# Kernel optimization log

Measured on AMD Instinct MI355X. Metric: run time of the kernel, lower is better.

Reference implementation:

```python
import jax, jax.numpy as jnp
import numpy as np

EPS = 1e-6
HQ, HKV, HD = 16, 4, 64   # num_q_heads, num_kv_heads, head_dim
TOPK = 2                  # num_exp_tokens
B, S, H, E, I = 2, 1024, 1024, 8, 2048


def _rms(x, w):
    return x * jax.lax.rsqrt(jnp.mean(x * x, -1, keepdims=True) + EPS) * w


def _rope(x, cos, sin):
    # x: [B,S,h,D]; cos/sin: [S,D/2]
    x1, x2 = jnp.split(x, 2, axis=-1)
    c = cos[None, :, None, :]
    s = sin[None, :, None, :]
    return jnp.concatenate([x1 * c - x2 * s, x1 * s + x2 * c], axis=-1)


def setup_inputs() -> dict:
    key = jax.random.key(0)
    ks = jax.random.split(key, 12)
    w = lambda k, sh: jax.random.normal(k, sh, jnp.float32) * 0.02
    return {
        "x": jax.random.normal(ks[0], (B, S, H), jnp.float32),
        "freq": jax.random.uniform(ks[1], (S, HD // 2), jnp.float32) * 6.28,
        "norm1_w": jnp.ones((H,), jnp.float32),
        "norm2_w": jnp.ones((H,), jnp.float32),
        "wq": w(ks[2], (H, HQ * HD)),
        "wk": w(ks[3], (H, HKV * HD)),
        "wv": w(ks[4], (H, HKV * HD)),
        "wo": w(ks[5], (HQ * HD, H)),
        "qn_w": jnp.ones((HD,), jnp.float32),
        "kn_w": jnp.ones((HD,), jnp.float32),
        "gate_w": w(ks[6], (H, E)),
        "w1": w(ks[7], (E, H, I)),
        "w2": w(ks[8], (E, I, H)),
        "w3": w(ks[9], (E, H, I)),
    }


def reference(x, freq, norm1_w, norm2_w, wq, wk, wv, wo, qn_w, kn_w,
              gate_w, w1, w2, w3):
    b, s, h = x.shape
    # ---- GQA attention with qk_norm + RoPE ----
    hn = _rms(x, norm1_w)
    q = (hn @ wq).reshape(b, s, HQ, HD)
    k = (hn @ wk).reshape(b, s, HKV, HD)
    v = (hn @ wv).reshape(b, s, HKV, HD)
    q = _rms(q, qn_w)
    k = _rms(k, kn_w)
    cos, sin = jnp.cos(freq), jnp.sin(freq)
    q = _rope(q, cos, sin)
    k = _rope(k, cos, sin)
    rep = HQ // HKV
    kr = jnp.repeat(k, rep, axis=2)  # [b,s,HQ,HD]
    vr = jnp.repeat(v, rep, axis=2)
    scores = jnp.einsum('bqhd,bkhd->bhqk', q, kr) * (HD ** -0.5)
    mask = jnp.tril(jnp.ones((s, s), bool))
    scores = jnp.where(mask, scores, jnp.finfo(scores.dtype).min)
    att = jax.nn.softmax(scores, axis=-1)
    y = jnp.einsum('bhqk,bkhd->bqhd', att, vr).reshape(b, s, HQ * HD) @ wo
    x = x + y

    # ---- Sparse MoE FFN (top-k softmax gate, SwiGLU experts) ----
    t = _rms(x, norm2_w).reshape(b * s, h)
    probs = jax.nn.softmax(t @ gate_w, axis=-1)          # [T,E]
    vals, idx = jax.lax.top_k(probs, TOPK)               # [T,k]
    vals = vals / jnp.sum(vals, -1, keepdims=True)       # renormalize top-k
    T = b * s
    combine = jnp.zeros((T, E), t.dtype).at[
        jnp.arange(T)[:, None], idx].add(vals)           # [T,E]
    u = jnp.einsum('th,ehi->eti', t, w1)
    g = jax.nn.silu(u) * jnp.einsum('th,ehi->eti', t, w3)
    ye = jnp.einsum('eti,eih->eth', g, w2)               # [E,T,H]
    moe = jnp.einsum('eth,te->th', ye, combine).reshape(b, s, h)
    return (x + moe, k, v)
```

## Files before the change

kernel.cpp:

```cpp
#include <hip/hip_runtime.h>
#include <hip/hip_bf16.h>

#define HQn 16
#define HKVn 4
#define HDn 64
#define Bn 2
#define Sn 1024
#define Hn 1024
#define En 8
#define In 2048
#define Tn 2048
#define EPSf 1e-6f

typedef __attribute__((ext_vector_type(8))) short bf16x8;
typedef __attribute__((ext_vector_type(4))) float f32x4;

__device__ __forceinline__ unsigned short f2bf(float f) {
  unsigned u = __float_as_uint(f);
  u += 0x7fffu + ((u >> 16) & 1u);
  return (unsigned short)(u >> 16);
}
__device__ __forceinline__ float bf2f(unsigned short u) {
  return __uint_as_float(((unsigned)u) << 16);
}
// ... 72 lines not shown
    unsigned short* __restrict__ outh, unsigned short* __restrict__ outl) {
  int row = blockIdx.x, tid = threadIdx.x;
  size_t off = (size_t)row * Hn + tid * 4;
  float4 v = *(const float4*)(x + off);
  float ss = v.x * v.x + v.y * v.y + v.z * v.z + v.w * v.w;
#pragma unroll
  for (int o = 32; o > 0; o >>= 1) ss += __shfl_xor(ss, o);
  __shared__ float ls[4];
  if ((tid & 63) == 0) ls[tid >> 6] = ss;
  __syncthreads();
  float tot = ls[0] + ls[1] + ls[2] + ls[3];
  float sc = rsqrtf(tot * (1.0f / Hn) + EPSf);
  float4 wv = *(const float4*)(w + tid * 4);
  float o0 = v.x * sc * wv.x, o1 = v.y * sc * wv.y;
  float o2 = v.z * sc * wv.z, o3 = v.w * sc * wv.w;
  ushort4 h4, l4;
  h4.x = f2bf(o0); l4.x = f2bf(o0 - bf2f(h4.x));
  h4.y = f2bf(o1); l4.y = f2bf(o1 - bf2f(h4.y));
  h4.z = f2bf(o2); l4.z = f2bf(o2 - bf2f(h4.z));
  h4.w = f2bf(o3); l4.w = f2bf(o3 - bf2f(h4.w));
  *(ushort4*)(outh + off) = h4;
  *(ushort4*)(outl + off) = l4;
}

__global__ __launch_bounds__(256) void k_resid_norm(
    const float* __restrict__ x, const float* __restrict__ y,
    const float* __restrict__ w, float* __restrict__ x2out,
    float* __restrict__ tout, unsigned short* __restrict__ tbf) {
  int row = blockIdx.x, tid = threadIdx.x;
  size_t off = (size_t)row * Hn + tid * 4;
  float4 xv = *(const float4*)(x + off);
  float4 yv = *(const float4*)(y + off);
  float4 s;
  s.x = xv.x + yv.x; s.y = xv.y + yv.y; s.z = xv.z + yv.z; s.w = xv.w + yv.w;
  *(float4*)(x2out + off) = s;
  float ss = s.x * s.x + s.y * s.y + s.z * s.z + s.w * s.w;
#pragma unroll
  for (int o = 32; o > 0; o >>= 1) ss += __shfl_xor(ss, o);
  __shared__ float ls[4];
  if ((tid & 63) == 0) ls[tid >> 6] = ss;
  __syncthreads();
  float tot = ls[0] + ls[1] + ls[2] + ls[3];
  float sc = rsqrtf(tot * (1.0f / Hn) + EPSf);
  float4 wv4 = *(const float4*)(w + tid * 4);
  float4 t4;
  t4.x = s.x * sc * wv4.x; t4.y = s.y * sc * wv4.y;
  t4.z = s.z * sc * wv4.z; t4.w = s.w * sc * wv4.w;
  *(float4*)(tout + off) = t4;
  ushort4 b4;
  b4.x = f2bf(t4.x); b4.y = f2bf(t4.y); b4.z = f2bf(t4.z); b4.w = f2bf(t4.w);
  *(ushort4*)(tbf + off) = b4;
}

template<int MT>
__global__ __launch_bounds__(256) void k_pgemm(
    const unsigned short* __restrict__ Ah, const unsigned short* __restrict__ Al,
    const unsigned short* __restrict__ Bth, const unsigned short* __restrict__ Btl,
    float* __restrict__ C, int N, int K) {
  constexpr int BM = MT * 32;
  __shared__ __align__(16) short smAh[BM * 32], smAl[BM * 32];
  __shared__ __align__(16) short smBh[4096], smBl[4096];
  int tid = threadIdx.x, wave = tid >> 6, lane = tid & 63;
  int n0 = blockIdx.x * 128, m0 = blockIdx.y * BM;
  int wm = wave >> 1, wn = wave & 1;
  int r0 = ((tid >> 6) << 4) | (tid & 15);
  int k0 = ((tid >> 4) & 3) * 8;
  int r1 = r0 + 64;
  const unsigned short* Ah0 = Ah + (size_t)(m0 + r0) * K + k0;
  const unsigned short* Al0 = Al + (size_t)(m0 + r0) * K + k0;
  const unsigned short* Bh0 = Bth + (size_t)(n0 + r0) * K + k0;
  const unsigned short* Bl0 = Btl + (size_t)(n0 + r0) * K + k0;
  const unsigned short* Bh1 = Bth + (size_t)(n0 + r1) * K + k0;
  const unsigned short* Bl1 = Btl + (size_t)(n0 + r1) * K + k0;
  short* dA0h = smAh + (size_t)(wave * 64) * 8;
  short* dA0l = smAl + (size_t)(wave * 64) * 8;
  short* dB0h = smBh + (size_t)(wave * 64) * 8;
  short* dB0l = smBl + (size_t)(wave * 64) * 8;
  short* dB1h = smBh + (size_t)(256 + wave * 64) * 8;
  short* dB1l = smBl + (size_t)(256 + wave * 64) * 8;
  const unsigned short* Ah1 = Ah0;
  const unsigned short* Al1 = Al0;
  short* dA1h = smAh;
  short* dA1l = smAl;
  if constexpr (MT == 4) {
    Ah1 = Ah + (size_t)(m0 + r1) * K + k0;
    Al1 = Al + (size_t)(m0 + r1) * K + k0;
    dA1h = smAh + (size_t)(256 + wave * 64) * 8;
    dA1l = smAl + (size_t)(256 + wave * 64) * 8;
  }
  f32x4 zf = {0.f, 0.f, 0.f, 0.f};
  f32x4 acc[MT][4];
#pragma unroll
  for (int i = 0; i < MT; i++)
#pragma unroll
    for (int j = 0; j < 4; j++) acc[i][j] = zf;
  for (int kb = 0; kb < K; kb += 32) {
    __syncthreads();
    gll16(Ah0 + kb, dA0h);
    gll16(Al0 + kb, dA0l);
    if constexpr (MT == 4) {
      gll16(Ah1 + kb, dA1h);
      gll16(Al1 + kb, dA1l);
    }
    gll16(Bh0 + kb, dB0h);
    gll16(Bl0 + kb, dB0l);
    gll16(Bh1 + kb, dB1h);
    gll16(Bl1 + kb, dB1l);
    __syncthreads();
    bf16x8 ah[MT], al[MT], bh[4], bl[4];
#pragma unroll
    for (int i = 0; i < MT; i++) {
      ah[i] = *(const bf16x8*)(smAh + ((wm * MT + i) * 64 + lane) * 8);
      al[i] = *(const bf16x8*)(smAl + ((wm * MT + i) * 64 + lane) * 8);
    }
#pragma unroll
    for (int j = 0; j < 4; j++) {
      bh[j] = *(const bf16x8*)(smBh + ((wn * 4 + j) * 64 + lane) * 8);
      bl[j] = *(const bf16x8*)(smBl + ((wn * 4 + j) * 64 + lane) * 8);
    }
#pragma unroll
    for (int i = 0; i < MT; i++)
#pragma unroll
      for (int j = 0; j < 4; j++) {
        acc[i][j] = __builtin_amdgcn_mfma_f32_16x16x32_bf16(ah[i], bh[j], acc[i][j], 0, 0, 0);
        acc[i][j] = __builtin_amdgcn_mfma_f32_16x16x32_bf16(ah[i], bl[j], acc[i][j], 0, 0, 0);
        acc[i][j] = __builtin_amdgcn_mfma_f32_16x16x32_bf16(al[i], bh[j], acc[i][j], 0, 0, 0);
      }
  }
  int cr = (lane >> 4) * 4, cc = lane & 15;
#pragma unroll
  for (int i = 0; i < MT; i++) {
    int row0 = m0 + (wm * MT + i) * 16 + cr;
#pragma unroll
    for (int j = 0; j < 4; j++) {
      int col = n0 + (wn * 4 + j) * 16 + cc;
#pragma unroll
      for (int r = 0; r < 4; r++)
        C[(size_t)(row0 + r) * N + col] = acc[i][j][r];
    }
  }
}

__global__ __launch_bounds__(256) void k_qkv_post(
    const float* __restrict__ qkv, const float* __restrict__ qn_w,
    const float* __restrict__ kn_w, const float* __restrict__ freq,
    float* __restrict__ q_t,
    unsigned short* __restrict__ kT8h, unsigned short* __restrict__ kT8l,
    unsigned short* __restrict__ vT8h, unsigned short* __restrict__ vT8l,
    float* __restrict__ k_out, float* __restrict__ v_out) {
  int gw = blockIdx.x * 4 + (threadIdx.x >> 6);
  int lane = threadIdx.x & 63;
  int token = gw / 24;
  int hh = gw % 24;
  int b = token / Sn, s = token % Sn;
  if (hh >= 20) {
    int h = hh - 20;
    float v = qkv[(size_t)token * 1536 + 1280 + h * HDn + lane];
    unsigned short hi = f2bf(v);
    unsigned short lo = f2bf(v - bf2f(hi));
    size_t vb = (((size_t)(b * HKVn + h) * 128 + (s >> 3)) * 64 + lane) * 8 + (s & 7);
    vT8h[vb] = hi; vT8l[vb] = lo;
    v_out[(size_t)token * (HKVn * HDn) + h * HDn + lane] = v;
    return;
  }
  bool isq = hh < 16;
  int h = isq ? hh : hh - 16;
  float val = isq ? qkv[(size_t)token * 1536 + h * HDn + lane]
                  : qkv[(size_t)token * 1536 + 1024 + h * HDn + lane];
  float ss = val * val;
#pragma unroll
  for (int o = 32; o > 0; o >>= 1) ss += __shfl_xor(ss, o);
  float scn = rsqrtf(ss * (1.0f / HDn) + EPSf);
  float w = isq ? qn_w[lane] : kn_w[lane];
  float xn = val * scn * w;
  float f = freq[(size_t)s * (HDn / 2) + (lane & 31)];
  float c = cosf(f), sn = sinf(f);
  float partner = __shfl_xor(xn, 32);
  float out = (lane < 32) ? (xn * c - partner * sn) : (partner * sn + xn * c);
  if (isq) {
    q_t[(((size_t)(b * HQn + h)) * Sn + s) * HDn + lane] = out;
  } else {
    unsigned short hi = f2bf(out);
    unsigned short lo = f2bf(out - bf2f(hi));
    size_t kb = (((size_t)(b * HKVn + h) * 8 + (lane >> 3)) * Sn + s) * 8 + (lane & 7);
    kT8h[kb] = hi; kT8l[kb] = lo;
// ... 154 lines not shown
    s[6] = fmaf(tv, g1.z, s[6]); s[7] = fmaf(tv, g1.w, s[7]);
  }
#pragma unroll
  for (int e = 0; e < 8; e++)
#pragma unroll
    for (int off = 32; off > 0; off >>= 1) s[e] += __shfl_xor(s[e], off);
  if (lane == 0) {
    float mx = s[0];
    for (int e = 1; e < 8; e++) mx = fmaxf(mx, s[e]);
    float p[8];
    for (int e = 0; e < 8; e++) p[e] = __expf(s[e] - mx);
    int e0 = 0;
    for (int e = 1; e < 8; e++) if (p[e] > p[e0]) e0 = e;
    int e1 = (e0 == 0) ? 1 : 0;
    for (int e = 0; e < 8; e++) if (e != e0 && p[e] > p[e1]) e1 = e;
    float v0 = p[e0], v1 = p[e1], inv = 1.f / (v0 + v1);
    idx[tok * 2] = e0; idx[tok * 2 + 1] = e1;
    val[tok * 2] = v0 * inv; val[tok * 2 + 1] = v1 * inv;
    atomicAdd(&cnt[e0], 1); atomicAdd(&cnt[e1], 1);
  }
}

__global__ void k_scan(const int* __restrict__ cnt, int* __restrict__ offs,
                       int* __restrict__ cursor) {
  if (threadIdx.x == 0) {
    int run = 0;
    for (int e = 0; e < En; e++) { offs[e] = run; cursor[e] = run; run += cnt[e]; }
  }
}

__global__ __launch_bounds__(256) void k_scatter(
    const int* __restrict__ idx, const float* __restrict__ val,
    int* __restrict__ cursor, int* __restrict__ tokl, float* __restrict__ wvl) {
  int t = blockIdx.x * 256 + threadIdx.x;
#pragma unroll
  for (int slot = 0; slot < 2; slot++) {
    int e = idx[t * 2 + slot];
    int pos = atomicAdd(&cursor[e], 1);
    tokl[pos] = t;
    wvl[pos] = val[t * 2 + slot];
  }
}

__global__ __launch_bounds__(256) void k_gather(
    const unsigned short* __restrict__ tb, const int* __restrict__ tokl,
    unsigned short* __restrict__ tg) {
  int r = blockIdx.x;
  int tk = tokl[r];
  const ushort4* s = (const ushort4*)(tb + (size_t)tk * Hn);
  ushort4* d = (ushort4*)(tg + (size_t)r * Hn);
  d[threadIdx.x] = s[threadIdx.x];
}

__global__ __launch_bounds__(256) void k_moe13(
    const unsigned short* __restrict__ tg, const unsigned short* __restrict__ w13t,
    unsigned short* __restrict__ ug, const int* __restrict__ cnt,
    const int* __restrict__ offs) {
  int e = blockIdx.z;
  int n_e = cnt[e];
  int mt = blockIdx.y;
  if (mt * 128 >= n_e) return;
  int base = offs[e];
  const unsigned short* A = tg + (size_t)(base + mt * 128) * Hn;
  const unsigned short* Bt = w13t + (size_t)e * (2 * In) * Hn;
  __shared__ __align__(16) short smA[4096];
  __shared__ __align__(16) short smB[4096];
  int tid = threadIdx.x;
  int wave = tid >> 6, lane = tid & 63;
  int n0 = blockIdx.x * 128;
  int wm = wave >> 1, wn = wave & 1;
  int s0 = tid, s1 = 256 + tid;
  int r0s = ((s0 >> 6) << 4) | (s0 & 15), k0s = ((s0 >> 4) & 3) * 8;
  int r1s = ((s1 >> 6) << 4) | (s1 & 15), k1s = ((s1 >> 4) & 3) * 8;
  const unsigned short* Ap0 = A + (size_t)r0s * Hn + k0s;
  const unsigned short* Ap1 = A + (size_t)r1s * Hn + k1s;
  const unsigned short* Bp0 = Bt + (size_t)(n0 + r0s) * Hn + k0s;
  const unsigned short* Bp1 = Bt + (size_t)(n0 + r1s) * Hn + k1s;
  short* lA0 = smA + (size_t)(wave * 64) * 8;
  short* lA1 = smA + (size_t)(256 + wave * 64) * 8;
  short* lB0 = smB + (size_t)(wave * 64) * 8;
  short* lB1 = smB + (size_t)(256 + wave * 64) * 8;
  f32x4 zf = {0.f, 0.f, 0.f, 0.f};
  f32x4 acc[4][4];
#pragma unroll
  for (int i = 0; i < 4; i++)
#pragma unroll
    for (int j = 0; j < 4; j++) acc[i][j] = zf;
  for (int kb = 0; kb < Hn; kb += 32) {
    __syncthreads();
    gll16(Ap0 + kb, lA0);
    gll16(Ap1 + kb, lA1);
    gll16(Bp0 + kb, lB0);
    gll16(Bp1 + kb, lB1);
    __syncthreads();
    bf16x8 af[4], bfr[4];
#pragma unroll
    for (int i = 0; i < 4; i++)
      af[i] = *(const bf16x8*)(smA + ((wm * 4 + i) * 64 + lane) * 8);
#pragma unroll
    for (int j = 0; j < 4; j++)
      bfr[j] = *(const bf16x8*)(smB + ((wn * 4 + j) * 64 + lane) * 8);
#pragma unroll
    for (int i = 0; i < 4; i++)
#pragma unroll
      for (int j = 0; j < 4; j++)
        acc[i][j] = __builtin_amdgcn_mfma_f32_16x16x32_bf16(af[i], bfr[j], acc[i][j], 0, 0, 0);
  }
  int cr = (lane >> 4) * 4, cc = lane & 15;
#pragma unroll
  for (int i = 0; i < 4; i++) {
    int lrow0 = (wm * 4 + i) * 16 + cr;
#pragma unroll
    for (int j = 0; j < 4; j++) {
      int ncol = n0 + (wn * 4 + j) * 16 + cc;
#pragma unroll
      for (int r = 0; r < 4; r++) {
        int rr = mt * 128 + lrow0 + r;
        if (rr < n_e)
          ug[(size_t)(base + rr) * (2 * In) + ncol] = f2bf(acc[i][j][r]);
      }
    }
  }
}

__global__ __launch_bounds__(256) void k_act(
    const unsigned short* __restrict__ ug, unsigned short* __restrict__ act) {
  size_t p = ((size_t)blockIdx.x * 256 + threadIdx.x) * 8;
  size_t r = p >> 11;
  int c = (int)(p & 2047);
  const ushort4* up = (const ushort4*)(ug + r * 4096 + c);
  const ushort4* gp = (const ushort4*)(ug + r * 4096 + 2048 + c);
  ushort4* ap = (ushort4*)(act + r * 2048 + c);
#pragma unroll
  for (int h = 0; h < 2; h++) {
    ushort4 uu = up[h], gg = gp[h];
    ushort4 oo;
    float u0 = bf2f(uu.x), u1 = bf2f(uu.y), u2 = bf2f(uu.z), u3 = bf2f(uu.w);
    oo.x = f2bf(u0 / (1.f + __expf(-u0)) * bf2f(gg.x));
    oo.y = f2bf(u1 / (1.f + __expf(-u1)) * bf2f(gg.y));
    oo.z = f2bf(u2 / (1.f + __expf(-u2)) * bf2f(gg.z));
    oo.w = f2bf(u3 / (1.f + __expf(-u3)) * bf2f(gg.w));
    ap[h] = oo;
  }
}

__global__ __launch_bounds__(256) void k_moe2(
    const unsigned short* __restrict__ act, const unsigned short* __restrict__ w2t,
    const int* __restrict__ cnt, const int* __restrict__ offs,
    const int* __restrict__ tokl, const float* __restrict__ wvl,
    float* __restrict__ out0) {
  int e = blockIdx.z;
  int n_e = cnt[e];
  int mt = blockIdx.y;
  if (mt * 128 >= n_e) return;
  int base = offs[e];
  __shared__ int ltok[128];
  __shared__ float lwv[128];
  int tid = threadIdx.x;
  if (tid < 128) {
    int rr = mt * 128 + tid;
    bool v = rr < n_e;
    ltok[tid] = v ? tokl[base + rr] : -1;
    lwv[tid] = v ? wvl[base + rr] : 0.f;
  }
  const unsigned short* A = act + (size_t)(base + mt * 128) * In;
  const unsigned short* Bt = w2t + (size_t)e * Hn * In;
  __shared__ __align__(16) short smA[4096];
  __shared__ __align__(16) short smB[4096];
  int wave = tid >> 6, lane = tid & 63;
  int n0 = blockIdx.x * 128;
  int wm = wave >> 1, wn = wave & 1;
  int s0 = tid, s1 = 256 + tid;
  int r0s = ((s0 >> 6) << 4) | (s0 & 15), k0s = ((s0 >> 4) & 3) * 8;
  int r1s = ((s1 >> 6) << 4) | (s1 & 15), k1s = ((s1 >> 4) & 3) * 8;
  const unsigned short* Ap0 = A + (size_t)r0s * In + k0s;
  const unsigned short* Ap1 = A + (size_t)r1s * In + k1s;
  const unsigned short* Bp0 = Bt + (size_t)(n0 + r0s) * In + k0s;
  const unsigned short* Bp1 = Bt + (size_t)(n0 + r1s) * In + k1s;
  short* lA0 = smA + (size_t)(wave * 64) * 8;
  short* lA1 = smA + (size_t)(256 + wave * 64) * 8;
  short* lB0 = smB + (size_t)(wave * 64) * 8;
  short* lB1 = smB + (size_t)(256 + wave * 64) * 8;
  f32x4 zf = {0.f, 0.f, 0.f, 0.f};
  f32x4 acc[4][4];
#pragma unroll
  for (int i = 0; i < 4; i++)
#pragma unroll
    for (int j = 0; j < 4; j++) acc[i][j] = zf;
  for (int kb = 0; kb < In; kb += 32) {
    __syncthreads();
    gll16(Ap0 + kb, lA0);
    gll16(Ap1 + kb, lA1);
    gll16(Bp0 + kb, lB0);
    gll16(Bp1 + kb, lB1);
    __syncthreads();
    bf16x8 af[4], bfr[4];
#pragma unroll
    for (int i = 0; i < 4; i++)
      af[i] = *(const bf16x8*)(smA + ((wm * 4 + i) * 64 + lane) * 8);
#pragma unroll
    for (int j = 0; j < 4; j++)
      bfr[j] = *(const bf16x8*)(smB + ((wn * 4 + j) * 64 + lane) * 8);
#pragma unroll
    for (int i = 0; i < 4; i++)
#pragma unroll
      for (int j = 0; j < 4; j++)
        acc[i][j] = __builtin_amdgcn_mfma_f32_16x16x32_bf16(af[i], bfr[j], acc[i][j], 0, 0, 0);
  }
  int cr = (lane >> 4) * 4, cc = lane & 15;
#pragma unroll
  for (int i = 0; i < 4; i++) {
    int lrow0 = (wm * 4 + i) * 16 + cr;
#pragma unroll
    for (int j = 0; j < 4; j++) {
      int ncol = n0 + (wn * 4 + j) * 16 + cc;
#pragma unroll
      for (int r = 0; r < 4; r++) {
        int lrow = lrow0 + r;
        int tk = ltok[lrow];
        if (tk >= 0)
          atomicAdd(out0 + (size_t)tk * Hn + ncol, lwv[lrow] * acc[i][j][r]);
      }
    }
  }
}

extern "C" void kernel_launch(void* const* d_in, const int* in_sizes, int n_in,
                              void* d_out, int out_size, void* d_ws, size_t ws_size,
                              hipStream_t stream) {
  (void)in_sizes; (void)n_in; (void)out_size; (void)ws_size;
  const float* x      = (const float*)d_in[0];
  const float* freq   = (const float*)d_in[1];
  const float* n1w    = (const float*)d_in[2];
  const float* n2w    = (const float*)d_in[3];
  const float* wq     = (const float*)d_in[4];
  const float* wk     = (const float*)d_in[5];
  const float* wvp    = (const float*)d_in[6];
  const float* wo     = (const float*)d_in[7];
  const float* qn_w   = (const float*)d_in[8];
  const float* kn_w   = (const float*)d_in[9];
  const float* gate_w = (const float*)d_in[10];
  const float* w1     = (const float*)d_in[11];
  const float* w2     = (const float*)d_in[12];
  const float* w3     = (const float*)d_in[13];

  float* out0  = (float*)d_out;
  float* k_out = out0 + (size_t)Tn * Hn;
  float* v_out = k_out + (size_t)Tn * HKVn * HDn;

  char* wsb = (char*)d_ws;
  unsigned short* w13t = (unsigned short*)(wsb + 0);
  unsigned short* w2t  = (unsigned short*)(wsb + 67108864);
  unsigned short* tbf  = (unsigned short*)(wsb + 100663296);
  unsigned short* tg   = (unsigned short*)(wsb + 104857600);
  unsigned short* wqkvt_h = (unsigned short*)(wsb + 113246208);
  unsigned short* wqkvt_l = (unsigned short*)(wsb + 116391936);
  unsigned short* wot_h   = (unsigned short*)(wsb + 119537664);
  unsigned short* wot_l   = (unsigned short*)(wsb + 121634816);
  unsigned short* act  = (unsigned short*)(wsb + 113246208);
  unsigned short* hnh  = (unsigned short*)(wsb + 130023424);
  unsigned short* hnl  = (unsigned short*)(wsb + 134217728);
  float* qkv_raw = (float*)(wsb + 138412032);
  float* q_t   = (float*)(wsb + 150994944);
  unsigned short* kT8h = (unsigned short*)(wsb + 159383552);
  unsigned short* kT8l = (unsigned short*)(wsb + 160432128);
  unsigned short* vT8h = (unsigned short*)(wsb + 161480704);
  unsigned short* vT8l = (unsigned short*)(wsb + 162529280);
  unsigned short* ug = (unsigned short*)(wsb + 130023424);
  unsigned short* yh = (unsigned short*)(wsb + 163577856);
  unsigned short* yl = (unsigned short*)(wsb + 167772160);
  float* y2    = (float*)(wsb + 171966464);
  float* t_norm = (float*)(wsb + 150994944);
  char*  rtr   = wsb + 180355072;
  int*   idxb   = (int*)(rtr);
  float* valb   = (float*)(rtr + 16384);
  int*   cnt    = (int*)(rtr + 32768);
  int*   offs   = (int*)(rtr + 32768 + 128);
  int*   cursor = (int*)(rtr + 32768 + 256);
  int*   tokl   = (int*)(rtr + 32768 + 384);
  float* wvl    = (float*)(rtr + 32768 + 384 + 16384);

  k_tcvt<<<dim3(32, 16, 8), 256, 0, stream>>>(w1, w13t, 1024, 2048,
                                              (size_t)1024 * 2048, (size_t)4096 * 1024);
  k_tcvt<<<dim3(32, 16, 8), 256, 0, stream>>>(w3, w13t + (size_t)2048 * 1024, 1024, 2048,
                                              (size_t)1024 * 2048, (size_t)4096 * 1024);
  k_tcvt<<<dim3(16, 32, 8), 256, 0, stream>>>(w2, w2t, 2048, 1024,
                                              (size_t)2048 * 1024, (size_t)1024 * 2048);
  k_tcvt2<<<dim3(16, 16), 256, 0, stream>>>(wq, wqkvt_h, wqkvt_l, 1024, 1024);
  k_tcvt2<<<dim3(4, 16), 256, 0, stream>>>(wk, wqkvt_h + (size_t)1024 * 1024,
                                           wqkvt_l + (size_t)1024 * 1024, 1024, 256);
  k_tcvt2<<<dim3(4, 16), 256, 0, stream>>>(wvp, wqkvt_h + (size_t)1280 * 1024,
                                           wqkvt_l + (size_t)1280 * 1024, 1024, 256);
  k_tcvt2<<<dim3(16, 16), 256, 0, stream>>>(wo, wot_h, wot_l, 1024, 1024);

  hipMemsetAsync(cnt, 0, 8 * sizeof(int), stream);

  k_rmsnorm<<<Tn, 256, 0, stream>>>(x, n1w, hnh, hnl);
  k_pgemm<4><<<dim3(12, 16), 256, 0, stream>>>(hnh, hnl, wqkvt_h, wqkvt_l,
                                               qkv_raw, 1536, 1024);
  k_qkv_post<<<(Tn * 24) / 4, 256, 0, stream>>>(qkv_raw, qn_w, kn_w,
                                                freq, q_t, kT8h, kT8l, vT8h, vT8l,
                                                k_out, v_out);
  k_attn_mfma<<<Bn * HKVn * 64, 256, 0, stream>>>(q_t, kT8h, kT8l, vT8h, vT8l, yh, yl);
  k_pgemm<2><<<dim3(8, 32), 256, 0, stream>>>(yh, yl, wot_h, wot_l, y2, 1024, 1024);
  k_resid_norm<<<Tn, 256, 0, stream>>>(x, y2, n2w, out0, t_norm, tbf);
  k_router<<<Tn / 4, 256, 0, stream>>>(t_norm, gate_w, idxb, valb, cnt);
  k_scan<<<1, 64, 0, stream>>>(cnt, offs, cursor);
  k_scatter<<<Tn / 256, 256, 0, stream>>>(idxb, valb, cursor, tokl, wvl);
  k_gather<<<2 * Tn, 256, 0, stream>>>(tbf, tokl, tg);
  k_moe13<<<dim3(32, 16, 8), 256, 0, stream>>>(tg, w13t, ug, cnt, offs);
  k_act<<<4096, 256, 0, stream>>>(ug, act);
  k_moe2<<<dim3(8, 16, 8), 256, 0, stream>>>(act, w2t, cnt, offs, tokl, wvl, out0);
}
```

Baseline: 712.3 us.

## Double-buffer LDS in GEMM kernels and widen MoE blocks to 512 threads

Adds two-stage LDS double buffering to the split-precision projection GEMM and both MoE expert GEMMs. The next K-slice is issued into the alternate buffer while MFMAs run on the current one, which drops one barrier per iteration. The MoE kernels also move to 512-thread blocks: moe13 covers 256 token rows per block, and moe2 gives each wave a 32x64 sub-tile. The cost is more LDS per block and different wave-to-tile mappings, which may lower occupancy, and it relies on the global-to-LDS loads completing before the trailing barrier.

After: 680.6 us. -4.5%, faster.

```diff
diff --git a/kernel.cpp b/kernel.cpp
--- a/kernel.cpp
+++ b/kernel.cpp
@@ -154,65 +154,61 @@
     const unsigned short* __restrict__ Bth, const unsigned short* __restrict__ Btl,
     float* __restrict__ C, int N, int K) {
   constexpr int BM = MT * 32;
-  __shared__ __align__(16) short smAh[BM * 32], smAl[BM * 32];
-  __shared__ __align__(16) short smBh[4096], smBl[4096];
+  constexpr int ASL = BM * 32;
+  __shared__ __align__(16) short smAh[2][ASL], smAl[2][ASL];
+  __shared__ __align__(16) short smBh[2][4096], smBl[2][4096];
   int tid = threadIdx.x, wave = tid >> 6, lane = tid & 63;
   int n0 = blockIdx.x * 128, m0 = blockIdx.y * BM;
   int wm = wave >> 1, wn = wave & 1;
   int r0 = ((tid >> 6) << 4) | (tid & 15);
   int k0 = ((tid >> 4) & 3) * 8;
   int r1 = r0 + 64;
-  const unsigned short* Ah0 = Ah + (size_t)(m0 + r0) * K + k0;
-  const unsigned short* Al0 = Al + (size_t)(m0 + r0) * K + k0;
-  const unsigned short* Bh0 = Bth + (size_t)(n0 + r0) * K + k0;
-  const unsigned short* Bl0 = Btl + (size_t)(n0 + r0) * K + k0;
-  const unsigned short* Bh1 = Bth + (size_t)(n0 + r1) * K + k0;
-  const unsigned short* Bl1 = Btl + (size_t)(n0 + r1) * K + k0;
-  short* dA0h = smAh + (size_t)(wave * 64) * 8;
-  short* dA0l = smAl + (size_t)(wave * 64) * 8;
-  short* dB0h = smBh + (size_t)(wave * 64) * 8;
-  short* dB0l = smBl + (size_t)(wave * 64) * 8;
-  short* dB1h = smBh + (size_t)(256 + wave * 64) * 8;
-  short* dB1l = smBl + (size_t)(256 + wave * 64) * 8;
-  const unsigned short* Ah1 = Ah0;
-  const unsigned short* Al1 = Al0;
-  short* dA1h = smAh;
-  short* dA1l = smAl;
+  const unsigned short* pAh0 = Ah + (size_t)(m0 + r0) * K + k0;
+  const unsigned short* pAl0 = Al + (size_t)(m0 + r0) * K + k0;
+  const unsigned short* pBh0 = Bth + (size_t)(n0 + r0) * K + k0;
+  const unsigned short* pBl0 = Btl + (size_t)(n0 + r0) * K + k0;
+  const unsigned short* pBh1 = Bth + (size_t)(n0 + r1) * K + k0;
+  const unsigned short* pBl1 = Btl + (size_t)(n0 + r1) * K + k0;
+  const unsigned short* pAh1 = pAh0;
+  const unsigned short* pAl1 = pAl0;
   if constexpr (MT == 4) {
-    Ah1 = Ah + (size_t)(m0 + r1) * K + k0;
-    Al1 = Al + (size_t)(m0 + r1) * K + k0;
-    dA1h = smAh + (size_t)(256 + wave * 64) * 8;
-    dA1l = smAl + (size_t)(256 + wave * 64) * 8;
-  }
+    pAh1 = Ah + (size_t)(m0 + r1) * K + k0;
+    pAl1 = Al + (size_t)(m0 + r1) * K + k0;
+  }
+  int d0 = tid * 8, d1 = (256 + tid) * 8;
+  auto STAGE = [&](int b, int kb) {
+    gll16(pAh0 + kb, &smAh[b][d0]);
+    gll16(pAl0 + kb, &smAl[b][d0]);
+    if constexpr (MT == 4) {
+      gll16(pAh1 + kb, &smAh[b][d1]);
+      gll16(pAl1 + kb, &smAl[b][d1]);
+    }
+    gll16(pBh0 + kb, &smBh[b][d0]);
+    gll16(pBl0 + kb, &smBl[b][d0]);
+    gll16(pBh1 + kb, &smBh[b][d1]);
+    gll16(pBl1 + kb, &smBl[b][d1]);
+  };
   f32x4 zf = {0.f, 0.f, 0.f, 0.f};
   f32x4 acc[MT][4];
 #pragma unroll
   for (int i = 0; i < MT; i++)
 #pragma unroll
     for (int j = 0; j < 4; j++) acc[i][j] = zf;
+  STAGE(0, 0);
+  __syncthreads();
   for (int kb = 0; kb < K; kb += 32) {
-    __syncthreads();
-    gll16(Ah0 + kb, dA0h);
-    gll16(Al0 + kb, dA0l);
-    if constexpr (MT == 4) {
-      gll16(Ah1 + kb, dA1h);
-      gll16(Al1 + kb, dA1l);
-    }
-    gll16(Bh0 + kb, dB0h);
-    gll16(Bl0 + kb, dB0l);
-    gll16(Bh1 + kb, dB1h);
-    gll16(Bl1 + kb, dB1l);
-    __syncthreads();
+    int cur = (kb >> 5) & 1;
+    if (kb + 32 < K) STAGE(cur ^ 1, kb + 32);
     bf16x8 ah[MT], al[MT], bh[4], bl[4];
 #pragma unroll
     for (int i = 0; i < MT; i++) {
-      ah[i] = *(const bf16x8*)(smAh + ((wm * MT + i) * 64 + lane) * 8);
-      al[i] = *(const bf16x8*)(smAl + ((wm * MT + i) * 64 + lane) * 8);
+      ah[i] = *(const bf16x8*)&smAh[cur][((wm * MT + i) * 64 + lane) * 8];
+      al[i] = *(const bf16x8*)&smAl[cur][((wm * MT + i) * 64 + lane) * 8];
     }
 #pragma unroll
     for (int j = 0; j < 4; j++) {
-      bh[j] = *(const bf16x8*)(smBh + ((wn * 4 + j) * 64 + lane) * 8);
-      bl[j] = *(const bf16x8*)(smBl + ((wn * 4 + j) * 64 + lane) * 8);
+      bh[j] = *(const bf16x8*)&smBh[cur][((wn * 4 + j) * 64 + lane) * 8];
+      bl[j] = *(const bf16x8*)&smBl[cur][((wn * 4 + j) * 64 + lane) * 8];
     }
 #pragma unroll
     for (int i = 0; i < MT; i++)
@@ -222,6 +218,7 @@
         acc[i][j] = __builtin_amdgcn_mfma_f32_16x16x32_bf16(ah[i], bl[j], acc[i][j], 0, 0, 0);
         acc[i][j] = __builtin_amdgcn_mfma_f32_16x16x32_bf16(al[i], bh[j], acc[i][j], 0, 0, 0);
       }
+    __syncthreads();
   }
   int cr = (lane >> 4) * 4, cc = lane & 15;
 #pragma unroll
@@ -487,70 +484,68 @@
   d[threadIdx.x] = s[threadIdx.x];
 }
 
-__global__ __launch_bounds__(256) void k_moe13(
+__global__ __launch_bounds__(512) void k_moe13(
     const unsigned short* __restrict__ tg, const unsigned short* __restrict__ w13t,
     unsigned short* __restrict__ ug, const int* __restrict__ cnt,
     const int* __restrict__ offs) {
   int e = blockIdx.z;
   int n_e = cnt[e];
   int mt = blockIdx.y;
-  if (mt * 128 >= n_e) return;
+  if (mt * 256 >= n_e) return;
   int base = offs[e];
-  const unsigned short* A = tg + (size_t)(base + mt * 128) * Hn;
+  const unsigned short* A = tg + (size_t)(base + mt * 256) * Hn;
   const unsigned short* Bt = w13t + (size_t)e * (2 * In) * Hn;
-  __shared__ __align__(16) short smA[4096];
-  __shared__ __align__(16) short smB[4096];
+  __shared__ __align__(16) short smA[2][8192];
+  __shared__ __align__(16) short smB[2][4096];
   int tid = threadIdx.x;
   int wave = tid >> 6, lane = tid & 63;
   int n0 = blockIdx.x * 128;
   int wm = wave >> 1, wn = wave & 1;
-  int s0 = tid, s1 = 256 + tid;
-  int r0s = ((s0 >> 6) << 4) | (s0 & 15), k0s = ((s0 >> 4) & 3) * 8;
-  int r1s = ((s1 >> 6) << 4) | (s1 & 15), k1s = ((s1 >> 4) & 3) * 8;
-  const unsigned short* Ap0 = A + (size_t)r0s * Hn + k0s;
-  const unsigned short* Ap1 = A + (size_t)r1s * Hn + k1s;
-  const unsigned short* Bp0 = Bt + (size_t)(n0 + r0s) * Hn + k0s;
-  const unsigned short* Bp1 = Bt + (size_t)(n0 + r1s) * Hn + k1s;
-  short* lA0 = smA + (size_t)(wave * 64) * 8;
-  short* lA1 = smA + (size_t)(256 + wave * 64) * 8;
-  short* lB0 = smB + (size_t)(wave * 64) * 8;
-  short* lB1 = smB + (size_t)(256 + wave * 64) * 8;
+  int r0s = ((tid >> 6) << 4) | (tid & 15);
+  int k0s = ((tid >> 4) & 3) * 8;
+  const unsigned short* ApA = A + (size_t)r0s * Hn + k0s;
+  const unsigned short* ApB = A + (size_t)(r0s + 128) * Hn + k0s;
+  const unsigned short* BpB = Bt + (size_t)(n0 + r0s) * Hn + k0s;
+  auto STAGE = [&](int b, int kb) {
+    gll16(ApA + kb, &smA[b][tid * 8]);
+    gll16(ApB + kb, &smA[b][(512 + tid) * 8]);
+    gll16(BpB + kb, &smB[b][tid * 8]);
+  };
   f32x4 zf = {0.f, 0.f, 0.f, 0.f};
   f32x4 acc[4][4];
 #pragma unroll
   for (int i = 0; i < 4; i++)
 #pragma unroll
     for (int j = 0; j < 4; j++) acc[i][j] = zf;
+  STAGE(0, 0);
+  __syncthreads();
   for (int kb = 0; kb < Hn; kb += 32) {
-    __syncthreads();
-    gll16(Ap0 + kb, lA0);
-    gll16(Ap1 + kb, lA1);
-    gll16(Bp0 + kb, lB0);
-    gll16(Bp1 + kb, lB1);
-    __syncthreads();
+    int cur = (kb >> 5) & 1;
+    if (kb + 32 < Hn) STAGE(cur ^ 1, kb + 32);
     bf16x8 af[4], bfr[4];
 #pragma unroll
     for (int i = 0; i < 4; i++)
-      af[i] = *(const bf16x8*)(smA + ((wm * 4 + i) * 64 + lane) * 8);
+      af[i] = *(const bf16x8*)&smA[cur][((wm * 4 + i) * 64 + lane) * 8];
 #pragma unroll
     for (int j = 0; j < 4; j++)
-      bfr[j] = *(const bf16x8*)(smB + ((wn * 4 + j) * 64 + lane) * 8);
+      bfr[j] = *(const bf16x8*)&smB[cur][((wn * 4 + j) * 64 + lane) * 8];
 #pragma unroll
     for (int i = 0; i < 4; i++)
 #pragma unroll
       for (int j = 0; j < 4; j++)
         acc[i][j] = __builtin_amdgcn_mfma_f32_16x16x32_bf16(af[i], bfr[j], acc[i][j], 0, 0, 0);
+    __syncthreads();
   }
   int cr = (lane >> 4) * 4, cc = lane & 15;
 #pragma unroll
   for (int i = 0; i < 4; i++) {
-    int lrow0 = (wm * 4 + i) * 16 + cr;
+    int lrow0 = wm * 64 + i * 16 + cr;
 #pragma unroll
     for (int j = 0; j < 4; j++) {
-      int ncol = n0 + (wn * 4 + j) * 16 + cc;
+      int ncol = n0 + wn * 64 + j * 16 + cc;
 #pragma unroll
       for (int r = 0; r < 4; r++) {
-        int rr = mt * 128 + lrow0 + r;
+        int rr = mt * 256 + lrow0 + r;
         if (rr < n_e)
           ug[(size_t)(base + rr) * (2 * In) + ncol] = f2bf(acc[i][j][r]);
       }
@@ -579,7 +574,7 @@
   }
 }
 
-__global__ __launch_bounds__(256) void k_moe2(
+__global__ __launch_bounds__(512) void k_moe2(
     const unsigned short* __restrict__ act, const unsigned short* __restrict__ w2t,
     const int* __restrict__ cnt, const int* __restrict__ offs,
     const int* __restrict__ tokl, const float* __restrict__ wvl,
@@ -600,55 +595,51 @@
   }
   const unsigned short* A = act + (size_t)(base + mt * 128) * In;
   const unsigned short* Bt = w2t + (size_t)e * Hn * In;
-  __shared__ __align__(16) short smA[4096];
-  __shared__ __align__(16) short smB[4096];
+  __shared__ __align__(16) short smA[2][4096];
+  __shared__ __align__(16) short smB[2][4096];
   int wave = tid >> 6, lane = tid & 63;
   int n0 = blockIdx.x * 128;
   int wm = wave >> 1, wn = wave & 1;
-  int s0 = tid, s1 = 256 + tid;
-  int r0s = ((s0 >> 6) << 4) | (s0 & 15), k0s = ((s0 >> 4) & 3) * 8;
-  int r1s = ((s1 >> 6) << 4) | (s1 & 15), k1s = ((s1 >> 4) & 3) * 8;
-  const unsigned short* Ap0 = A + (size_t)r0s * In + k0s;
-  const unsigned short* Ap1 = A + (size_t)r1s * In + k1s;
-  const unsigned short* Bp0 = Bt + (size_t)(n0 + r0s) * In + k0s;
-  const unsigned short* Bp1 = Bt + (size_t)(n0 + r1s) * In + k1s;
-  short* lA0 = smA + (size_t)(wave * 64) * 8;
-  short* lA1 = smA + (size_t)(256 + wave * 64) * 8;
-  short* lB0 = smB + (size_t)(wave * 64) * 8;
-  short* lB1 = smB + (size_t)(256 + wave * 64) * 8;
+  int r0s = ((tid >> 6) << 4) | (tid & 15);
+  int k0s = ((tid >> 4) & 3) * 8;
+  const unsigned short* ApA = A + (size_t)r0s * In + k0s;
+  const unsigned short* BpB = Bt + (size_t)(n0 + r0s) * In + k0s;
+  auto STAGE = [&](int b, int kb) {
+    gll16(ApA + kb, &smA[b][tid * 8]);
+    gll16(BpB + kb, &smB[b][tid * 8]);
+  };
   f32x4 zf = {0.f, 0.f, 0.f, 0.f};
-  f32x4 acc[4][4];
-#pragma unroll
-  for (int i = 0; i < 4; i++)
+  f32x4 acc[2][4];
+#pragma unroll
+  for (int i = 0; i < 2; i++)
 #pragma unroll
     for (int j = 0; j < 4; j++) acc[i][j] = zf;
+  STAGE(0, 0);
+  __syncthreads();
   for (int kb = 0; kb < In; kb += 32) {
-    __syncthreads();
-    gll16(Ap0 + kb, lA0);
-    gll16(Ap1 + kb, lA1);
-    gll16(Bp0 + kb, lB0);
-    gll16(Bp1 + kb, lB1);
-    __syncthreads();
-    bf16x8 af[4], bfr[4];
-#pragma unroll
-    for (int i = 0; i < 4; i++)
-      af[i] = *(const bf16x8*)(smA + ((wm * 4 + i) * 64 + lane) * 8);
+    int cur = (kb >> 5) & 1;
+    if (kb + 32 < In) STAGE(cur ^ 1, kb + 32);
+    bf16x8 af[2], bfr[4];
+#pragma unroll
+    for (int i = 0; i < 2; i++)
+      af[i] = *(const bf16x8*)&smA[cur][((wm * 2 + i) * 64 + lane) * 8];
 #pragma unroll
     for (int j = 0; j < 4; j++)
-      bfr[j] = *(const bf16x8*)(smB + ((wn * 4 + j) * 64 + lane) * 8);
-#pragma unroll
-    for (int i = 0; i < 4; i++)
+      bfr[j] = *(const bf16x8*)&smB[cur][((wn * 4 + j) * 64 + lane) * 8];
+#pragma unroll
+    for (int i = 0; i < 2; i++)
 #pragma unroll
       for (int j = 0; j < 4; j++)
         acc[i][j] = __builtin_amdgcn_mfma_f32_16x16x32_bf16(af[i], bfr[j], acc[i][j], 0, 0, 0);
+    __syncthreads();
   }
   int cr = (lane >> 4) * 4, cc = lane & 15;
 #pragma unroll
-  for (int i = 0; i < 4; i++) {
-    int lrow0 = (wm * 4 + i) * 16 + cr;
+  for (int i = 0; i < 2; i++) {
+    int lrow0 = wm * 32 + i * 16 + cr;
 #pragma unroll
     for (int j = 0; j < 4; j++) {
-      int ncol = n0 + (wn * 4 + j) * 16 + cc;
+      int ncol = n0 + wn * 64 + j * 16 + cc;
 #pragma unroll
       for (int r = 0; r < 4; r++) {
         int lrow = lrow0 + r;
@@ -743,7 +734,7 @@
   k_scan<<<1, 64, 0, stream>>>(cnt, offs, cursor);
   k_scatter<<<Tn / 256, 256, 0, stream>>>(idxb, valb, cursor, tokl, wvl);
   k_gather<<<2 * Tn, 256, 0, stream>>>(tbf, tokl, tg);
-  k_moe13<<<dim3(32, 16, 8), 256, 0, stream>>>(tg, w13t, ug, cnt, offs);
+  k_moe13<<<dim3(32, 8, 8), 512, 0, stream>>>(tg, w13t, ug, cnt, offs);
   k_act<<<4096, 256, 0, stream>>>(ug, act);
-  k_moe2<<<dim3(8, 16, 8), 256, 0, stream>>>(act, w2t, cnt, offs, tokl, wvl, out0);
-}
+  k_moe2<<<dim3(8, 16, 8), 512, 0, stream>>>(act, w2t, cnt, offs, tokl, wvl, out0);
+}
```

## Double-buffer LDS tiles in GEMM kernels to overlap global loads with MFMA

Applied to the files above, without the earlier changes.

Adds double-buffered shared-memory staging to the split-bf16 projection GEMM and both MoE expert GEMMs. The next K-slice is loaded while the current one is computed, which halves the number of barriers per K step and hides load latency. The projection GEMM also drops its template and always uses a 64-row M tile, so the QKV launch doubles its grid. The cost is twice the LDS per block, which may reduce occupancy.

After: 698.7 us. Within noise of the previous version (-1.9%).

```diff
diff --git a/kernel.cpp b/kernel.cpp
--- a/kernel.cpp
+++ b/kernel.cpp
@@ -148,85 +148,76 @@
   *(ushort4*)(tbf + off) = b4;
 }
 
-template<int MT>
 __global__ __launch_bounds__(256) void k_pgemm(
     const unsigned short* __restrict__ Ah, const unsigned short* __restrict__ Al,
     const unsigned short* __restrict__ Bth, const unsigned short* __restrict__ Btl,
     float* __restrict__ C, int N, int K) {
-  constexpr int BM = MT * 32;
-  __shared__ __align__(16) short smAh[BM * 32], smAl[BM * 32];
-  __shared__ __align__(16) short smBh[4096], smBl[4096];
+  __shared__ __align__(16) short sAh0[2048], sAh1[2048], sAl0[2048], sAl1[2048];
+  __shared__ __align__(16) short sBh0[4096], sBh1[4096], sBl0[4096], sBl1[4096];
   int tid = threadIdx.x, wave = tid >> 6, lane = tid & 63;
-  int n0 = blockIdx.x * 128, m0 = blockIdx.y * BM;
+  int n0 = blockIdx.x * 128, m0 = blockIdx.y * 64;
   int wm = wave >> 1, wn = wave & 1;
   int r0 = ((tid >> 6) << 4) | (tid & 15);
   int k0 = ((tid >> 4) & 3) * 8;
   int r1 = r0 + 64;
-  const unsigned short* Ah0 = Ah + (size_t)(m0 + r0) * K + k0;
-  const unsigned short* Al0 = Al + (size_t)(m0 + r0) * K + k0;
-  const unsigned short* Bh0 = Bth + (size_t)(n0 + r0) * K + k0;
-  const unsigned short* Bl0 = Btl + (size_t)(n0 + r0) * K + k0;
-  const unsigned short* Bh1 = Bth + (size_t)(n0 + r1) * K + k0;
-  const unsigned short* Bl1 = Btl + (size_t)(n0 + r1) * K + k0;
-  short* dA0h = smAh + (size_t)(wave * 64) * 8;
-  short* dA0l = smAl + (size_t)(wave * 64) * 8;
-  short* dB0h = smBh + (size_t)(wave * 64) * 8;
-  short* dB0l = smBl + (size_t)(wave * 64) * 8;
-  short* dB1h = smBh + (size_t)(256 + wave * 64) * 8;
-  short* dB1l = smBl + (size_t)(256 + wave * 64) * 8;
-  const unsigned short* Ah1 = Ah0;
-  const unsigned short* Al1 = Al0;
-  short* dA1h = smAh;
-  short* dA1l = smAl;
-  if constexpr (MT == 4) {
-    Ah1 = Ah + (size_t)(m0 + r1) * K + k0;
-    Al1 = Al + (size_t)(m0 + r1) * K + k0;
-    dA1h = smAh + (size_t)(256 + wave * 64) * 8;
-    dA1l = smAl + (size_t)(256 + wave * 64) * 8;
-  }
+  const unsigned short* pAh = Ah + (size_t)(m0 + r0) * K + k0;
+  const unsigned short* pAl = Al + (size_t)(m0 + r0) * K + k0;
+  const unsigned short* pBh0 = Bth + (size_t)(n0 + r0) * K + k0;
+  const unsigned short* pBl0 = Btl + (size_t)(n0 + r0) * K + k0;
+  const unsigned short* pBh1 = Bth + (size_t)(n0 + r1) * K + k0;
+  const unsigned short* pBl1 = Btl + (size_t)(n0 + r1) * K + k0;
+  size_t d0 = (size_t)tid * 8, d1 = (size_t)(256 + tid) * 8;
+#define PG_STAGE(S, kb) do { \
+    gll16(pAh + (kb), sAh##S + d0); \
+    gll16(pAl + (kb), sAl##S + d0); \
+    gll16(pBh0 + (kb), sBh##S + d0); \
+    gll16(pBl0 + (kb), sBl##S + d0); \
+    gll16(pBh1 + (kb), sBh##S + d1); \
+    gll16(pBl1 + (kb), sBl##S + d1); \
+  } while (0)
+#define PG_COMP(S) do { \
+    bf16x8 ah[2], al[2], bh[4], bl[4]; \
+    _Pragma("unroll") \
+    for (int i = 0; i < 2; i++) { \
+      ah[i] = *(const bf16x8*)(sAh##S + ((wm * 2 + i) * 64 + lane) * 8); \
+      al[i] = *(const bf16x8*)(sAl##S + ((wm * 2 + i) * 64 + lane) * 8); \
+    } \
+    _Pragma("unroll") \
+    for (int j = 0; j < 4; j++) { \
+      bh[j] = *(const bf16x8*)(sBh##S + ((wn * 4 + j) * 64 + lane) * 8); \
+      bl[j] = *(const bf16x8*)(sBl##S + ((wn * 4 + j) * 64 + lane) * 8); \
+    } \
+    _Pragma("unroll") \
+    for (int i = 0; i < 2; i++) \
+      _Pragma("unroll") \
+      for (int j = 0; j < 4; j++) { \
+        acc[i][j] = __builtin_amdgcn_mfma_f32_16x16x32_bf16(ah[i], bh[j], acc[i][j], 0, 0, 0); \
+        acc[i][j] = __builtin_amdgcn_mfma_f32_16x16x32_bf16(ah[i], bl[j], acc[i][j], 0, 0, 0); \
+        acc[i][j] = __builtin_amdgcn_mfma_f32_16x16x32_bf16(al[i], bh[j], acc[i][j], 0, 0, 0); \
+      } \
+  } while (0)
   f32x4 zf = {0.f, 0.f, 0.f, 0.f};
-  f32x4 acc[MT][4];
-#pragma unroll
-  for (int i = 0; i < MT; i++)
+  f32x4 acc[2][4];
+#pragma unroll
+  for (int i = 0; i < 2; i++)
 #pragma unroll
     for (int j = 0; j < 4; j++) acc[i][j] = zf;
-  for (int kb = 0; kb < K; kb += 32) {
+  PG_STAGE(0, 0);
+  __syncthreads();
+  for (int kb = 0; kb < K; kb += 64) {
+    PG_STAGE(1, kb + 32);
+    PG_COMP(0);
     __syncthreads();
-    gll16(Ah0 + kb, dA0h);
-    gll16(Al0 + kb, dA0l);
-    if constexpr (MT == 4) {
-      gll16(Ah1 + kb, dA1h);
-      gll16(Al1 + kb, dA1l);
-    }
-    gll16(Bh0 + kb, dB0h);
-    gll16(Bl0 + kb, dB0l);
-    gll16(Bh1 + kb, dB1h);
-    gll16(Bl1 + kb, dB1l);
+    if (kb + 64 < K) PG_STAGE(0, kb + 64);
+    PG_COMP(1);
     __syncthreads();
-    bf16x8 ah[MT], al[MT], bh[4], bl[4];
-#pragma unroll
-    for (int i = 0; i < MT; i++) {
-      ah[i] = *(const bf16x8*)(smAh + ((wm * MT + i) * 64 + lane) * 8);
-      al[i] = *(const bf16x8*)(smAl + ((wm * MT + i) * 64 + lane) * 8);
-    }
-#pragma unroll
-    for (int j = 0; j < 4; j++) {
-      bh[j] = *(const bf16x8*)(smBh + ((wn * 4 + j) * 64 + lane) * 8);
-      bl[j] = *(const bf16x8*)(smBl + ((wn * 4 + j) * 64 + lane) * 8);
-    }
-#pragma unroll
-    for (int i = 0; i < MT; i++)
-#pragma unroll
-      for (int j = 0; j < 4; j++) {
-        acc[i][j] = __builtin_amdgcn_mfma_f32_16x16x32_bf16(ah[i], bh[j], acc[i][j], 0, 0, 0);
-        acc[i][j] = __builtin_amdgcn_mfma_f32_16x16x32_bf16(ah[i], bl[j], acc[i][j], 0, 0, 0);
-        acc[i][j] = __builtin_amdgcn_mfma_f32_16x16x32_bf16(al[i], bh[j], acc[i][j], 0, 0, 0);
-      }
-  }
+  }
+#undef PG_STAGE
+#undef PG_COMP
   int cr = (lane >> 4) * 4, cc = lane & 15;
 #pragma unroll
-  for (int i = 0; i < MT; i++) {
-    int row0 = m0 + (wm * MT + i) * 16 + cr;
+  for (int i = 0; i < 2; i++) {
+    int row0 = m0 + (wm * 2 + i) * 16 + cr;
 #pragma unroll
     for (int j = 0; j < 4; j++) {
       int col = n0 + (wn * 4 + j) * 16 + cc;
@@ -498,49 +489,57 @@
   int base = offs[e];
   const unsigned short* A = tg + (size_t)(base + mt * 128) * Hn;
   const unsigned short* Bt = w13t + (size_t)e * (2 * In) * Hn;
-  __shared__ __align__(16) short smA[4096];
-  __shared__ __align__(16) short smB[4096];
+  __shared__ __align__(16) short sA0[4096], sA1[4096];
+  __shared__ __align__(16) short sB0[4096], sB1[4096];
   int tid = threadIdx.x;
   int wave = tid >> 6, lane = tid & 63;
   int n0 = blockIdx.x * 128;
   int wm = wave >> 1, wn = wave & 1;
-  int s0 = tid, s1 = 256 + tid;
-  int r0s = ((s0 >> 6) << 4) | (s0 & 15), k0s = ((s0 >> 4) & 3) * 8;
-  int r1s = ((s1 >> 6) << 4) | (s1 & 15), k1s = ((s1 >> 4) & 3) * 8;
+  int r0s = ((tid >> 6) << 4) | (tid & 15), k0s = ((tid >> 4) & 3) * 8;
+  int r1s = r0s + 64;
   const unsigned short* Ap0 = A + (size_t)r0s * Hn + k0s;
-  const unsigned short* Ap1 = A + (size_t)r1s * Hn + k1s;
+  const unsigned short* Ap1 = A + (size_t)r1s * Hn + k0s;
   const unsigned short* Bp0 = Bt + (size_t)(n0 + r0s) * Hn + k0s;
-  const unsigned short* Bp1 = Bt + (size_t)(n0 + r1s) * Hn + k1s;
-  short* lA0 = smA + (size_t)(wave * 64) * 8;
-  short* lA1 = smA + (size_t)(256 + wave * 64) * 8;
-  short* lB0 = smB + (size_t)(wave * 64) * 8;
-  short* lB1 = smB + (size_t)(256 + wave * 64) * 8;
+  const unsigned short* Bp1 = Bt + (size_t)(n0 + r1s) * Hn + k0s;
+  size_t d0 = (size_t)tid * 8, d1 = (size_t)(256 + tid) * 8;
+#define M13_STAGE(S, kb) do { \
+    gll16(Ap0 + (kb), sA##S + d0); \
+    gll16(Ap1 + (kb), sA##S + d1); \
+    gll16(Bp0 + (kb), sB##S + d0); \
+    gll16(Bp1 + (kb), sB##S + d1); \
+  } while (0)
+#define M13_COMP(S) do { \
+    bf16x8 af[4], bfr[4]; \
+    _Pragma("unroll") \
+    for (int i = 0; i < 4; i++) \
+      af[i] = *(const bf16x8*)(sA##S + ((wm * 4 + i) * 64 + lane) * 8); \
+    _Pragma("unroll") \
+    for (int j = 0; j < 4; j++) \
+      bfr[j] = *(const bf16x8*)(sB##S + ((wn * 4 + j) * 64 + lane) * 8); \
+    _Pragma("unroll") \
+    for (int i = 0; i < 4; i++) \
+      _Pragma("unroll") \
+      for (int j = 0; j < 4; j++) \
+        acc[i][j] = __builtin_amdgcn_mfma_f32_16x16x32_bf16(af[i], bfr[j], acc[i][j], 0, 0, 0); \
+  } while (0)
   f32x4 zf = {0.f, 0.f, 0.f, 0.f};
   f32x4 acc[4][4];
 #pragma unroll
   for (int i = 0; i < 4; i++)
 #pragma unroll
     for (int j = 0; j < 4; j++) acc[i][j] = zf;
-  for (int kb = 0; kb < Hn; kb += 32) {
+  M13_STAGE(0, 0);
+  __syncthreads();
+  for (int kb = 0; kb < Hn; kb += 64) {
+    M13_STAGE(1, kb + 32);
+    M13_COMP(0);
     __syncthreads();
-    gll16(Ap0 + kb, lA0);
-    gll16(Ap1 + kb, lA1);
-    gll16(Bp0 + kb, lB0);
-    gll16(Bp1 + kb, lB1);
+    if (kb + 64 < Hn) M13_STAGE(0, kb + 64);
+    M13_COMP(1);
     __syncthreads();
-    bf16x8 af[4], bfr[4];
-#pragma unroll
-    for (int i = 0; i < 4; i++)
-      af[i] = *(const bf16x8*)(smA + ((wm * 4 + i) * 64 + lane) * 8);
-#pragma unroll
-    for (int j = 0; j < 4; j++)
-      bfr[j] = *(const bf16x8*)(smB + ((wn * 4 + j) * 64 + lane) * 8);
-#pragma unroll
-    for (int i = 0; i < 4; i++)
-#pragma unroll
-      for (int j = 0; j < 4; j++)
-        acc[i][j] = __builtin_amdgcn_mfma_f32_16x16x32_bf16(af[i], bfr[j], acc[i][j], 0, 0, 0);
-  }
+  }
+#undef M13_STAGE
+#undef M13_COMP
   int cr = (lane >> 4) * 4, cc = lane & 15;
 #pragma unroll
   for (int i = 0; i < 4; i++) {
@@ -600,48 +599,56 @@
   }
   const unsigned short* A = act + (size_t)(base + mt * 128) * In;
   const unsigned short* Bt = w2t + (size_t)e * Hn * In;
-  __shared__ __align__(16) short smA[4096];
-  __shared__ __align__(16) short smB[4096];
+  __shared__ __align__(16) short sA0[4096], sA1[4096];
+  __shared__ __align__(16) short sB0[4096], sB1[4096];
   int wave = tid >> 6, lane = tid & 63;
   int n0 = blockIdx.x * 128;
   int wm = wave >> 1, wn = wave & 1;
-  int s0 = tid, s1 = 256 + tid;
-  int r0s = ((s0 >> 6) << 4) | (s0 & 15), k0s = ((s0 >> 4) & 3) * 8;
-  int r1s = ((s1 >> 6) << 4) | (s1 & 15), k1s = ((s1 >> 4) & 3) * 8;
+  int r0s = ((tid >> 6) << 4) | (tid & 15), k0s = ((tid >> 4) & 3) * 8;
+  int r1s = r0s + 64;
   const unsigned short* Ap0 = A + (size_t)r0s * In + k0s;
-  const unsigned short* Ap1 = A + (size_t)r1s * In + k1s;
+  const unsigned short* Ap1 = A + (size_t)r1s * In + k0s;
   const unsigned short* Bp0 = Bt + (size_t)(n0 + r0s) * In + k0s;
-  const unsigned short* Bp1 = Bt + (size_t)(n0 + r1s) * In + k1s;
-  short* lA0 = smA + (size_t)(wave * 64) * 8;
-  short* lA1 = smA + (size_t)(256 + wave * 64) * 8;
-  short* lB0 = smB + (size_t)(wave * 64) * 8;
-  short* lB1 = smB + (size_t)(256 + wave * 64) * 8;
+  const unsigned short* Bp1 = Bt + (size_t)(n0 + r1s) * In + k0s;
+  size_t d0 = (size_t)tid * 8, d1 = (size_t)(256 + tid) * 8;
+#define M2_STAGE(S, kb) do { \
+    gll16(Ap0 + (kb), sA##S + d0); \
+    gll16(Ap1 + (kb), sA##S + d1); \
+    gll16(Bp0 + (kb), sB##S + d0); \
+    gll16(Bp1 + (kb), sB##S + d1); \
+  } while (0)
+#define M2_COMP(S) do { \
+    bf16x8 af[4], bfr[4]; \
+    _Pragma("unroll") \
+    for (int i = 0; i < 4; i++) \
+      af[i] = *(const bf16x8*)(sA##S + ((wm * 4 + i) * 64 + lane) * 8); \
+    _Pragma("unroll") \
+    for (int j = 0; j < 4; j++) \
+      bfr[j] = *(const bf16x8*)(sB##S + ((wn * 4 + j) * 64 + lane) * 8); \
+    _Pragma("unroll") \
+    for (int i = 0; i < 4; i++) \
+      _Pragma("unroll") \
+      for (int j = 0; j < 4; j++) \
+        acc[i][j] = __builtin_amdgcn_mfma_f32_16x16x32_bf16(af[i], bfr[j], acc[i][j], 0, 0, 0); \
+  } while (0)
   f32x4 zf = {0.f, 0.f, 0.f, 0.f};
   f32x4 acc[4][4];
 #pragma unroll
   for (int i = 0; i < 4; i++)
 #pragma unroll
     for (int j = 0; j < 4; j++) acc[i][j] = zf;
-  for (int kb = 0; kb < In; kb += 32) {
+  M2_STAGE(0, 0);
+  __syncthreads();
+  for (int kb = 0; kb < In; kb += 64) {
+    M2_STAGE(1, kb + 32);
+    M2_COMP(0);
     __syncthreads();
-    gll16(Ap0 + kb, lA0);
-    gll16(Ap1 + kb, lA1);
-    gll16(Bp0 + kb, lB0);
-    gll16(Bp1 + kb, lB1);
+    if (kb + 64 < In) M2_STAGE(0, kb + 64);
+    M2_COMP(1);
     __syncthreads();
-    bf16x8 af[4], bfr[4];
-#pragma unroll
-    for (int i = 0; i < 4; i++)
-      af[i] = *(const bf16x8*)(smA + ((wm * 4 + i) * 64 + lane) * 8);
-#pragma unroll
-    for (int j = 0; j < 4; j++)
-      bfr[j] = *(const bf16x8*)(smB + ((wn * 4 + j) * 64 + lane) * 8);
-#pragma unroll
-    for (int i = 0; i < 4; i++)
-#pragma unroll
-      for (int j = 0; j < 4; j++)
-        acc[i][j] = __builtin_amdgcn_mfma_f32_16x16x32_bf16(af[i], bfr[j], acc[i][j], 0, 0, 0);
-  }
+  }
+#undef M2_STAGE
+#undef M2_COMP
   int cr = (lane >> 4) * 4, cc = lane & 15;
 #pragma unroll
   for (int i = 0; i < 4; i++) {
@@ -731,13 +738,13 @@
   hipMemsetAsync(cnt, 0, 8 * sizeof(int), stream);
 
   k_rmsnorm<<<Tn, 256, 0, stream>>>(x, n1w, hnh, hnl);
-  k_pgemm<4><<<dim3(12, 16), 256, 0, stream>>>(hnh, hnl, wqkvt_h, wqkvt_l,
-                                               qkv_raw, 1536, 1024);
+  k_pgemm<<<dim3(12, 32), 256, 0, stream>>>(hnh, hnl, wqkvt_h, wqkvt_l,
+                                            qkv_raw, 1536, 1024);
   k_qkv_post<<<(Tn * 24) / 4, 256, 0, stream>>>(qkv_raw, qn_w, kn_w,
                                                 freq, q_t, kT8h, kT8l, vT8h, vT8l,
                                                 k_out, v_out);
   k_attn_mfma<<<Bn * HKVn * 64, 256, 0, stream>>>(q_t, kT8h, kT8l, vT8h, vT8l, yh, yl);
-  k_pgemm<2><<<dim3(8, 32), 256, 0, stream>>>(yh, yl, wot_h, wot_l, y2, 1024, 1024);
+  k_pgemm<<<dim3(8, 32), 256, 0, stream>>>(yh, yl, wot_h, wot_l, y2, 1024, 1024);
   k_resid_norm<<<Tn, 256, 0, stream>>>(x, y2, n2w, out0, t_norm, tbf);
   k_router<<<Tn / 4, 256, 0, stream>>>(t_norm, gate_w, idxb, valb, cnt);
   k_scan<<<1, 64, 0, stream>>>(cnt, offs, cursor);
```
